# Kernel optimization log

Hardware: AMD Instinct MI355X
Metric: run time of the kernel (lower is better)

The kernel has to match this reference:

```python
import jax, jax.numpy as jnp
import numpy as np

B, T, D, K, DEPTH = 8, 1024, 128, 64, 1


def _rel_ids(T, k):
    # relative_mat_id[i, j] = clamp(k + j - i, 0, 2k)
    base = jnp.arange(k, k + T)[None, :] - jnp.arange(T)[:, None]
    return jnp.clip(base, 0, 2 * k)  # [T, T] int32


def setup_inputs() -> dict:
    key = jax.random.key(0)
    ks = jax.random.split(key, 13)
    s = 1.0 / np.sqrt(D)
    return {
        "x": jax.random.normal(ks[0], (B, T, D), dtype=jnp.float32),
        "W0": jax.random.normal(ks[1], (D, D), dtype=jnp.float32) * s,
        "b0": jnp.zeros((D,), dtype=jnp.float32),
        "Wq": jax.random.normal(ks[2], (D, D), dtype=jnp.float32) * s,
        "bq": jnp.zeros((D,), dtype=jnp.float32),
        "Wk": jax.random.normal(ks[3], (D, D), dtype=jnp.float32) * s,
        "bk": jnp.zeros((D,), dtype=jnp.float32),
        "Wv": jax.random.normal(ks[4], (D, D), dtype=jnp.float32) * s,
        "bv": jnp.zeros((D,), dtype=jnp.float32),
        "W1": jax.random.normal(ks[5], (D, D), dtype=jnp.float32) * s,
        "b1": jnp.zeros((D,), dtype=jnp.float32),
        "pe_key": jax.random.normal(ks[6], (2 * K + 1, D), dtype=jnp.float32) * np.sqrt(2.0 / (2 * K + 1)),
        "pe_value": jax.random.normal(ks[7], (2 * K + 1, D), dtype=jnp.float32) * np.sqrt(2.0 / (2 * K + 1)),
    }


def reference(x, W0, b0, Wq, bq, Wk, bk, Wv, bv, W1, b1, pe_key, pe_value):
    Tlen = x.shape[1]
    ids = _rel_ids(Tlen, K)                     # [T, T]
    rpr_key = pe_key[ids]                       # [T, T, D]
    rpr_value = pe_value[ids]                   # [T, T, D]

    hs = jax.nn.relu(x @ W0 + b0)               # fc0 (dropout = eval identity)
    for _ in range(DEPTH):
        q = jnp.tanh(hs @ Wq + bq)
        k = jnp.tanh(hs @ Wk + bk)
        v = jnp.tanh(hs @ Wv + bv)
        a = jnp.einsum("bid,bjd->bij", q, k)
        a = a + jnp.einsum("ijd,bid->bij", rpr_key, q)
        a = jax.nn.softmax(a, axis=2)
        c = jnp.einsum("bij,bjd->bid", a, v)
        c = c + jnp.einsum("bij,ijd->bid", a, rpr_value)
        hs = jax.nn.relu(c @ W1 + b1)
    return hs
```

## Files before the change

kernel.cpp:

```cpp
#include <hip/hip_runtime.h>


#define TT 1024
#define DD 128
#define NB 8
#define SJH 1160

typedef _Float16 f16;
typedef __attribute__((ext_vector_type(8))) _Float16 f16x8;
typedef __attribute__((ext_vector_type(4))) _Float16 f16x4;
typedef __attribute__((ext_vector_type(4))) float f32x4;

static __device__ inline float fast_tanh(float x) {
    float xc = fminf(fmaxf(x, -12.f), 12.f);
    float e = __expf(2.f * xc);
    return (e - 1.f) / (e + 1.f);
}

#define GLDS(gp, lp) __builtin_amdgcn_global_load_lds( \
    (const __attribute__((address_space(1))) unsigned*)(gp), \
    (__attribute__((address_space(3))) unsigned*)(lp), 16, 0, 0)

__global__ __launch_bounds__(256) void prep_w(
        const float* __restrict__ W0, const float* __restrict__ Wq,
        const float* __restrict__ Wk, const float* __restrict__ Wv,
        const float* __restrict__ W1, char* __restrict__ wimg) {
    const int blk = blockIdx.x, t = threadIdx.x;
    const float* W = blk == 0 ? W0 : blk == 1 ? Wq : blk == 2 ? Wk
                   : blk == 3 ? Wv : W1;
    char* o = wimg + (size_t)blk * 32768;
    for (int it = 0; it < 64; it++) {
        int idx = t + 256 * it;
        int k = idx >> 7, n = idx & 127;
        int a = n * 256 + 2 * k;
        *(f16*)(o + (a ^ ((n & 7) << 4))) = (f16)W[k * 128 + n];
    }
}

#define ZACC() do { _Pragma("unroll") for (int _i = 0; _i < 2; _i++) \
    _Pragma("unroll") for (int _j = 0; _j < 2; _j++) \
        acc[_i][_j] = (f32x4){0.f, 0.f, 0.f, 0.f}; } while (0)

#define GEMMCORE(SRC, WL) do { \
    _Pragma("unroll") for (int _c = 0; _c < 4; _c++) { \
        f16x8 _af[2], _bf[2]; \
        _Pragma("unroll") for (int _it = 0; _it < 2; _it++) { \
            int _row = _it * 16 + (l & 15); \
            int _a = (_row << 8) + (_c << 6) + ((l >> 4) << 4); \
            _af[_it] = *(const f16x8*)((SRC) + (_a ^ ((_row & 7) << 4))); } \
        _Pragma("unroll") for (int _nt = 0; _nt < 2; _nt++) { \
            int _n = wv * 32 + _nt * 16 + (l & 15); \
            int _a = (_n << 8) + (_c << 6) + ((l >> 4) << 4); \
            _bf[_nt] = *(const f16x8*)((WL) + (_a ^ ((_n & 7) << 4))); } \
        _Pragma("unroll") for (int _it = 0; _it < 2; _it++) \
        _Pragma("unroll") for (int _nt = 0; _nt < 2; _nt++) \
            acc[_it][_nt] = __builtin_amdgcn_mfma_f32_16x16x32_f16( \
                    _af[_it], _bf[_nt], acc[_it][_nt], 0, 0, 0); } } while (0)

#define ISSUEW(wi, dst) do { \
    const char* _g = wimg + (size_t)(wi) * 32768 + t * 16; \
    char* _d = (dst) + t * 16; \
    _Pragma("unroll") for (int _i = 0; _i < 8; _i++) \
        GLDS(_g + _i * 4096, _d + _i * 4096); \
} while (0)

#define QKVBAR() do { \
    asm volatile("s_waitcnt vmcnt(0) lgkmcnt(0)" ::: "memory"); \
    __builtin_amdgcn_s_barrier(); \
    __builtin_amdgcn_sched_barrier(0); \
} while (0)

__global__ __launch_bounds__(256) void fused_qkv(
        const float* __restrict__ x, const char* __restrict__ wimg,
        const float* __restrict__ b0, const float* __restrict__ bq,
        const float* __restrict__ bk, const float* __restrict__ bv,
        const float* __restrict__ PEK, const float* __restrict__ PEV,
        f16* __restrict__ q16, char* __restrict__ kimg,
        char* __restrict__ vimg, char* __restrict__ pekimg,
        char* __restrict__ pevimg) {
    extern __shared__ __align__(16) char smq[];
    char* xs  = smq;
    char* hsl = smq + 8192;
    char* wA  = smq + 16384;
    char* wB  = smq + 49152;
    const int t = threadIdx.x, wv = t >> 6, l = t & 63;
    const int blk = blockIdx.x;

    if (blk >= 256) {
        if (blk == 256) {
            for (int it = 0; it < 64; it++) {
                int idx = t + 256 * it;
                int m = idx >> 7, d = idx & 127;
                *(f16*)(pekimg + (m >> 6) * 16384 + (m & 63) * 256
                        + ((2 * d) ^ ((m & 7) << 4))) = (f16)PEK[m * 128 + d];
            }
        } else {
            for (int it = 0; it < 64; it++) {
                int idx = t + 256 * it;
                int m = idx >> 7, d = idx & 127;
                *(f16*)(pevimg + (m >> 6) * 16384 + d * 128
                        + ((2 * (m & 63)) ^ ((d & 7) << 4))) = (f16)PEV[m * 128 + d];
            }
        }
        return;
    }

    const int r0 = blk * 32;
    ISSUEW(0, wA);
    {
        const float* X = x + (size_t)r0 * 128;
        #pragma unroll
        for (int i = 0; i < 2; i++) {
            f32x4 a0 = *(const f32x4*)(X + t * 16 + i * 8);
            f32x4 a1 = *(const f32x4*)(X + t * 16 + i * 8 + 4);
            f16x8 h;
            h[0]=(f16)a0[0]; h[1]=(f16)a0[1]; h[2]=(f16)a0[2]; h[3]=(f16)a0[3];
            h[4]=(f16)a1[0]; h[5]=(f16)a1[1]; h[6]=(f16)a1[2]; h[7]=(f16)a1[3];
            int a = t * 32 + i * 16;
            *(f16x8*)(xs + (a ^ (((a >> 8) & 7) << 4))) = h;
        }
    }
    QKVBAR();

    f32x4 acc[2][2];
    ISSUEW(1, wB);
    ZACC();
    GEMMCORE(xs, wA);
    {
        #pragma unroll
        for (int it = 0; it < 2; it++)
            #pragma unroll
            for (int nt = 0; nt < 2; nt++) {
                int n = wv * 32 + nt * 16 + (l & 15);
                float bb = b0[n];
                #pragma unroll
                for (int r = 0; r < 4; r++) {
                    int i = it * 16 + (l >> 4) * 4 + r;
                    float v = fmaxf(acc[it][nt][r] + bb, 0.f);
                    int a = i * 256 + 2 * n;
                    *(f16*)(hsl + (a ^ ((i & 7) << 4))) = (f16)v;
                }
            }
    }
    QKVBAR();

    ISSUEW(2, wA);
    ZACC();
    GEMMCORE(hsl, wB);
    {
        #pragma unroll
        for (int it = 0; it < 2; it++)
            #pragma unroll
            for (int nt = 0; nt < 2; nt++) {
                int n = wv * 32 + nt * 16 + (l & 15);
                float bb = bq[n];
                #pragma unroll
                for (int r = 0; r < 4; r++) {
                    int i = it * 16 + (l >> 4) * 4 + r;
                    q16[(size_t)(r0 + i) * 128 + n] =
                            (f16)fast_tanh(acc[it][nt][r] + bb);
                }
            }
    }
    QKVBAR();

    ISSUEW(3, wB);
    ZACC();
    GEMMCORE(hsl, wA);
    f16* ts = (f16*)xs;
    {
        #pragma unroll
        for (int it = 0; it < 2; it++)
            #pragma unroll
            for (int nt = 0; nt < 2; nt++) {
                int n = wv * 32 + nt * 16 + (l & 15);
                float bb = bk[n];
                #pragma unroll
                for (int r = 0; r < 4; r++) {
                    int i = it * 16 + (l >> 4) * 4 + r;
                    ts[i * 128 + n] = (f16)fast_tanh(acc[it][nt][r] + bb);
                }
            }
    }
    QKVBAR();

    {
        #pragma unroll
        for (int half = 0; half < 2; half++) {
            int row = (t >> 4) + half * 16;
            int seg = t & 15;
            int jg = r0 + row;
            int chunk = ((jg >> 10) << 4) + ((jg & 1023) >> 6);
            int jp = jg & 63;
            char* dst = kimg + (size_t)chunk * 16384 + jp * 256
                      + ((seg * 16) ^ ((jp & 7) << 4));
            *(f16x8*)dst = *(const f16x8*)&ts[row * 128 + seg * 8];
        }
    }
    ZACC();
    GEMMCORE(hsl, wB);
    {
        #pragma unroll
        for (int it = 0; it < 2; it++)
            #pragma unroll
            for (int nt = 0; nt < 2; nt++) {
                int d = wv * 32 + nt * 16 + (l & 15);
                float bb = bv[d];
                f16x4 h;
                #pragma unroll
                for (int r = 0; r < 4; r++)
                    h[r] = (f16)fast_tanh(acc[it][nt][r] + bb);
                int jb = r0 + it * 16 + ((l >> 4) << 2);
                int chunk = ((jb >> 10) << 4) + ((jb & 1023) >> 6);
                char* dst = vimg + (size_t)chunk * 16384 + d * 128
                          + ((2 * (jb & 63)) ^ ((d & 7) << 4));
                *(f16x4*)dst = h;
            }
    }
}

#define ISSUE16(src, bi) do { const char* _g = (src) + t * 16; \
    char* _d = BUF + (size_t)(bi) * 16384 + t * 16; \
    GLDS(_g, _d); \
    GLDS(_g + 8192, _d + 8192); \
} while (0)

__global__ __launch_bounds__(512) void attn_all(
        const f16* __restrict__ q16, const char* __restrict__ kimg,
        const char* __restrict__ pekimg, const char* __restrict__ vimg,
        const char* __restrict__ pevimg, const float* __restrict__ PEK,
        const float* __restrict__ PEV, const char* __restrict__ w1img,
        const float* __restrict__ b1, float* __restrict__ out) {
    extern __shared__ __align__(16) char sm7[];
    f16*   S   = (f16*)sm7;
    char*  BUF = sm7 + 74240;
    f16*   QB  = (f16*)(sm7 + 139776);
    float* LR  = (float*)(sm7 + 148224);

    const int t = threadIdx.x, wv = t >> 6, l = t & 63;
    const int lr = l & 15, lg = l >> 4;
    const int b = blockIdx.x & 7;
    const int i0 = (blockIdx.x >> 3) << 5;
    const int it16 = (wv & 1) << 4;
    const int jsub = wv >> 1;

    f16x8 qf[4];
    {
        const f16* qb = q16 + (size_t)(b * TT + i0 + it16 + lr) * 128 + lg * 8;
        #pragma unroll
        for (int c = 0; c < 4; c++) qf[c] = *(const f16x8*)(qb + c * 32);
    }
    const int row2 = t >> 4, l16 = t & 15;
    f16x8 qpv = *(const f16x8*)(q16 + (size_t)(b * TT + i0 + row2) * 128 + l16 * 8);
    f32x4 pkv0 = *(const f32x4*)(PEK + 128 * 128 + l16 * 8);
    f32x4 pkv1 = *(const f32x4*)(PEK + 128 * 128 + l16 * 8 + 4);
    f32x4 pvr4 = *(const f32x4*)(PEV + 128 * 128 + wv * 16 + lg * 4);
    const float bb1 = b1[wv * 16 + lr];

    const char* kbase = kimg + (size_t)b * 16 * 16384;
    const char* vbase = vimg + (size_t)b * 16 * 16384;

    ISSUE16(kbase, 0);
    ISSUE16(kbase + 16384, 1);
    ISSUE16(kbase + 2 * 16384, 2);

    for (int ch = 0; ch < 18; ch++) {
        asm volatile("s_waitcnt vmcnt(4)" ::: "memory");
        __builtin_amdgcn_s_barrier();
        __builtin_amdgcn_sched_barrier(0);
        {
            int ci = ch + 3;
            const char* src = ci < 16 ? kbase + (size_t)ci * 16384
                            : (ci < 18 ? pekimg + (size_t)(ci - 16) * 16384
                                       : vbase + (size_t)(ci - 18) * 16384);
            ISSUE16(src, ci & 3);
        }
        const char* kb = BUF + (size_t)(ch & 3) * 16384;
        const int jp = jsub * 16 + lr;
        f32x4 acc = {0.f, 0.f, 0.f, 0.f};
        #pragma unroll
        for (int c = 0; c < 4; c++) {
            f16x8 kf = *(const f16x8*)(kb + jp * 256
                        + ((c * 64 + lg * 16) ^ ((jp & 7) << 4)));
            acc = __builtin_amdgcn_mfma_f32_16x16x32_f16(kf, qf[c], acc, 0, 0, 0);
        }
        f16x4 h = {(f16)acc[0], (f16)acc[1], (f16)acc[2], (f16)acc[3]};
        *(f16x4*)&S[(it16 + lr) * SJH + ch * 64 + jsub * 16 + lg * 4] = h;
    }
    asm volatile("s_waitcnt lgkmcnt(0)" ::: "memory");
    __builtin_amdgcn_s_barrier();
    __builtin_amdgcn_sched_barrier(0);

    {
        const int ig = i0 + row2;
        f16* srow = S + row2 * SJH;
        f16* qrow = QB + row2 * 132;

        float qp;
        {
            float s = 0.f;
            #pragma unroll
            for (int e = 0; e < 4; e++) s += (float)qpv[e] * pkv0[e];
            #pragma unroll
            for (int e = 0; e < 4; e++) s += (float)qpv[e + 4] * pkv1[e];
            #pragma unroll
            for (int off = 8; off; off >>= 1) s += __shfl_xor(s, off, 64);
            qp = s;
        }
        for (int mm = l16; mm < 128; mm += 16) {
            qrow[mm] = srow[1024 + mm];
            srow[1024 + mm] = (f16)0.f;
        }
        if (l16 == 0) qrow[128] = (f16)qp;
        const float qlo = (float)qrow[0], qhi = qp;

        float lmax = -3.0e38f;
        #pragma unroll
        for (int kk = 0; kk < 8; kk++) {
            int j0 = kk * 128 + l16 * 8;
            f16x8 sv = *(const f16x8*)(srow + j0);
            #pragma unroll
            for (int e = 0; e < 8; e++) {
                int idd = 64 + j0 + e - ig;
                float qv = (idd <= 0) ? qlo : (idd >= 128 ? qhi : (float)qrow[idd]);
                lmax = fmaxf(lmax, (float)sv[e] + qv);
            }
        }
        #pragma unroll
        for (int off = 8; off; off >>= 1) lmax = fmaxf(lmax, __shfl_xor(lmax, off, 64));

        float lsum = 0.f, s0 = 0.f, s1 = 0.f;
        #pragma unroll
        for (int kk = 0; kk < 8; kk++) {
            int j0 = kk * 128 + l16 * 8;
            f16x8 sv = *(const f16x8*)(srow + j0);
            f16x8 pv;
            #pragma unroll
            for (int e = 0; e < 8; e++) {
                int idd = 64 + j0 + e - ig;
                float qv = (idd <= 0) ? qlo : (idd >= 128 ? qhi : (float)qrow[idd]);
                float p = __expf((float)sv[e] + qv - lmax);
                pv[e] = (f16)p;
                lsum += p;
                if (idd <= 0)        s0 += p;
                else if (idd >= 128) s1 += p;
                else                 srow[1024 + idd] = (f16)p;
            }
            *(f16x8*)(srow + j0) = pv;
        }
        #pragma unroll
        for (int off = 8; off; off >>= 1) {
            lsum += __shfl_xor(lsum, off, 64);
            s0   += __shfl_xor(s0,   off, 64);
            s1   += __shfl_xor(s1,   off, 64);
        }
        if (l16 == 0) {
            srow[1024] = (f16)s0;
            srow[1152] = (f16)s1;
            LR[row2] = lsum;
        }
    }
    asm volatile("s_waitcnt lgkmcnt(0)" ::: "memory");
    __builtin_amdgcn_s_barrier();
    __builtin_amdgcn_sched_barrier(0);

    f32x4 cacc[2] = {};
    for (int ch = 0; ch < 18; ch++) {
        if (ch <= 15)      asm volatile("s_waitcnt vmcnt(4)" ::: "memory");
        else if (ch == 16) asm volatile("s_waitcnt vmcnt(2)" ::: "memory");
        else               asm volatile("s_waitcnt vmcnt(0)" ::: "memory");
        __builtin_amdgcn_s_barrier();
        __builtin_amdgcn_sched_barrier(0);
        if (ch < 15) {
            int ci = ch + 3;
            const char* src = ci < 16 ? vbase + (size_t)ci * 16384
                                      : pevimg + (size_t)(ci - 16) * 16384;
            ISSUE16(src, (ci + 2) & 3);
        } else if (ch == 17) {
            const char* _g = w1img + t * 16;
            char* _d = BUF + t * 16;
            #pragma unroll
            for (int _i = 0; _i < 4; _i++)
                GLDS(_g + _i * 8192, _d + _i * 8192);
        }
        const char* vb = BUF + (size_t)((ch + 2) & 3) * 16384;
        const int dp = wv * 16 + lr;
        #pragma unroll
        for (int c2 = 0; c2 < 2; c2++) {
            f16x8 vf = *(const f16x8*)(vb + dp * 128
                        + ((c2 * 64 + lg * 16) ^ ((dp & 7) << 4)));
            #pragma unroll
            for (int i2 = 0; i2 < 2; i2++) {
                f16x8 pf = *(const f16x8*)&S[(i2 * 16 + lr) * SJH
                            + ch * 64 + c2 * 32 + lg * 8];
                cacc[i2] = __builtin_amdgcn_mfma_f32_16x16x32_f16(vf, pf, cacc[i2], 0, 0, 0);
            }
        }
    }

    float w128[2], rden[2];
    #pragma unroll
    for (int i2 = 0; i2 < 2; i2++) {
        int irow = i2 * 16 + lr;
        w128[i2] = (float)S[irow * SJH + 1152];
        rden[i2] = 1.f / LR[irow];
    }
    asm volatile("s_waitcnt lgkmcnt(0)" ::: "memory");
    __builtin_amdgcn_s_barrier();
    __builtin_amdgcn_sched_barrier(0);
    char* cl = (char*)S;
    {
        #pragma unroll
        for (int i2 = 0; i2 < 2; i2++) {
            int i = i2 * 16 + lr;
            #pragma unroll
            for (int r = 0; r < 4; r++) {
                int d = wv * 16 + lg * 4 + r;
                float cv = (cacc[i2][r] + w128[i2] * pvr4[r]) * rden[i2];
                int a = i * 256 + 2 * d;
                *(f16*)(cl + (a ^ ((i & 7) << 4))) = (f16)cv;
            }
        }
    }
    asm volatile("s_waitcnt vmcnt(0) lgkmcnt(0)" ::: "memory");
    __builtin_amdgcn_s_barrier();
    __builtin_amdgcn_sched_barrier(0);

    const char* wl4 = BUF;
    f32x4 oacc[2] = {};
    #pragma unroll
    for (int c = 0; c < 4; c++) {
        f16x8 af[2], bf;
        #pragma unroll
        for (int i2 = 0; i2 < 2; i2++) {
            int row = i2 * 16 + lr;
            int a = (row << 8) + (c << 6) + (lg << 4);
            af[i2] = *(const f16x8*)(cl + (a ^ ((row & 7) << 4)));
        }
        {
            int n = wv * 16 + lr;
            int a = (n << 8) + (c << 6) + (lg << 4);
            bf = *(const f16x8*)(wl4 + (a ^ ((n & 7) << 4)));
        }
        #pragma unroll
        for (int i2 = 0; i2 < 2; i2++)
            oacc[i2] = __builtin_amdgcn_mfma_f32_16x16x32_f16(af[i2], bf, oacc[i2], 0, 0, 0);
    }
    {
        int n = wv * 16 + lr;
        #pragma unroll
        for (int i2 = 0; i2 < 2; i2++) {
            #pragma unroll
            for (int r = 0; r < 4; r++) {
                int i = i2 * 16 + lg * 4 + r;
                out[(size_t)(b * TT + i0 + i) * DD + n] = fmaxf(oacc[i2][r] + bb1, 0.f);
            }
        }
    }
}


extern "C" void kernel_launch(void* const* d_in, const int* in_sizes, int n_in,
                              void* d_out, int out_size, void* d_ws, size_t ws_size,
                              hipStream_t stream) {
    const float* x   = (const float*)d_in[0];
    const float* W0  = (const float*)d_in[1];
    const float* b0  = (const float*)d_in[2];
    const float* Wq  = (const float*)d_in[3];
    const float* bq  = (const float*)d_in[4];
    const float* Wk  = (const float*)d_in[5];
    const float* bk  = (const float*)d_in[6];
    const float* Wv  = (const float*)d_in[7];
    const float* bv  = (const float*)d_in[8];
    const float* W1  = (const float*)d_in[9];
    const float* b1  = (const float*)d_in[10];
    const float* pek = (const float*)d_in[11];
    const float* pev = (const float*)d_in[12];
    float* out = (float*)d_out;

    const size_t NTD = (size_t)NB * TT * DD;
    f16* q16 = (f16*)d_ws;
    char* wimg   = (char*)(q16 + NTD);
    char* kimg   = wimg + 5 * 32768;
    char* vimg   = kimg + (size_t)128 * 16384;
    char* pekimg = vimg + (size_t)128 * 16384;
    char* pevimg = pekimg + 32768;

    const int SMEM_QKV  = 81920;
    const int SMEM_ATTN = 148352;
    hipFuncSetAttribute(reinterpret_cast<const void*>(fused_qkv),
                        hipFuncAttributeMaxDynamicSharedMemorySize, SMEM_QKV);
    hipFuncSetAttribute(reinterpret_cast<const void*>(attn_all),
                        hipFuncAttributeMaxDynamicSharedMemorySize, SMEM_ATTN);

    hipLaunchKernelGGL(prep_w, dim3(5), dim3(256), 0, stream,
                       W0, Wq, Wk, Wv, W1, wimg);
    hipLaunchKernelGGL(fused_qkv, dim3(258), dim3(256), SMEM_QKV, stream,
                       x, wimg, b0, bq, bk, bv, pek, pev,
                       q16, kimg, vimg, pekimg, pevimg);
    hipLaunchKernelGGL(attn_all, dim3(256), dim3(512), SMEM_ATTN, stream,
                       q16, kimg, pekimg, vimg, pevimg, pek, pev,
                       wimg + 4 * 32768, b1, out);
}
```

Before: 53.83 us.

## Triple-buffer weight loads in QKV kernel and vectorize weight prep

Adds a third LDS weight buffer so the next weight matrix is prefetched one stage further ahead, and replaces full vmcnt(0) waits with partial waits so async global-to-LDS loads overlap the GEMMs. It also remaps block-to-row assignment so consecutive blocks cover different batches, and vectorizes the prep_w kernel to write 8 halves per store. The cost is more LDS per block (114 KB), which may reduce occupancy, and the prep kernel's reads become strided.

Measured after the change: 51.82 us. -3.7%, faster.

```diff
diff --git a/kernel.cpp b/kernel.cpp
--- a/kernel.cpp
+++ b/kernel.cpp
@@ -29,11 +29,14 @@
     const float* W = blk == 0 ? W0 : blk == 1 ? Wq : blk == 2 ? Wk
                    : blk == 3 ? Wv : W1;
     char* o = wimg + (size_t)blk * 32768;
-    for (int it = 0; it < 64; it++) {
-        int idx = t + 256 * it;
-        int k = idx >> 7, n = idx & 127;
-        int a = n * 256 + 2 * k;
-        *(f16*)(o + (a ^ ((n & 7) << 4))) = (f16)W[k * 128 + n];
+    #pragma unroll
+    for (int it = 0; it < 8; it++) {
+        int item = t + 256 * it;
+        int n = item & 127, k0 = (item >> 7) * 8;
+        f16x8 h;
+        #pragma unroll
+        for (int e = 0; e < 8; e++) h[e] = (f16)W[(k0 + e) * 128 + n];
+        *(f16x8*)(o + n * 256 + ((2 * k0) ^ ((n & 7) << 4))) = h;
     }
 }
 
@@ -64,8 +67,8 @@
         GLDS(_g + _i * 4096, _d + _i * 4096); \
 } while (0)
 
-#define QKVBAR() do { \
-    asm volatile("s_waitcnt vmcnt(0) lgkmcnt(0)" ::: "memory"); \
+#define WAITBAR(N) do { \
+    asm volatile("s_waitcnt vmcnt(" #N ") lgkmcnt(0)" ::: "memory"); \
     __builtin_amdgcn_s_barrier(); \
     __builtin_amdgcn_sched_barrier(0); \
 } while (0)
@@ -83,6 +86,7 @@
     char* hsl = smq + 8192;
     char* wA  = smq + 16384;
     char* wB  = smq + 49152;
+    char* wC  = smq + 81920;
     const int t = threadIdx.x, wv = t >> 6, l = t & 63;
     const int blk = blockIdx.x;
 
@@ -105,8 +109,9 @@
         return;
     }
 
-    const int r0 = blk * 32;
+    const int r0 = (blk & 7) * 1024 + (blk >> 3) * 32;
     ISSUEW(0, wA);
+    ISSUEW(1, wB);
     {
         const float* X = x + (size_t)r0 * 128;
         #pragma unroll
@@ -120,10 +125,9 @@
             *(f16x8*)(xs + (a ^ (((a >> 8) & 7) << 4))) = h;
         }
     }
-    QKVBAR();
+    WAITBAR(8);
 
     f32x4 acc[2][2];
-    ISSUEW(1, wB);
     ZACC();
     GEMMCORE(xs, wA);
     {
@@ -142,9 +146,9 @@
                 }
             }
     }
-    QKVBAR();
-
-    ISSUEW(2, wA);
+    ISSUEW(2, wC);
+    WAITBAR(8);
+
     ZACC();
     GEMMCORE(hsl, wB);
     {
@@ -162,11 +166,11 @@
                 }
             }
     }
-    QKVBAR();
-
-    ISSUEW(3, wB);
+    ISSUEW(3, wA);
+    WAITBAR(8);
+
     ZACC();
-    GEMMCORE(hsl, wA);
+    GEMMCORE(hsl, wC);
     f16* ts = (f16*)xs;
     {
         #pragma unroll
@@ -182,7 +186,7 @@
                 }
             }
     }
-    QKVBAR();
+    WAITBAR(0);
 
     {
         #pragma unroll
@@ -198,7 +202,7 @@
         }
     }
     ZACC();
-    GEMMCORE(hsl, wB);
+    GEMMCORE(hsl, wA);
     {
         #pragma unroll
         for (int it = 0; it < 2; it++)
@@ -486,7 +490,7 @@
     char* pekimg = vimg + (size_t)128 * 16384;
     char* pevimg = pekimg + 32768;
 
-    const int SMEM_QKV  = 81920;
+    const int SMEM_QKV  = 114688;
     const int SMEM_ATTN = 148352;
     hipFuncSetAttribute(reinterpret_cast<const void*>(fused_qkv),
                         hipFuncAttributeMaxDynamicSharedMemorySize, SMEM_QKV);
```
